# Kernel tuning notes

Measured on AMD Instinct MI355X. Metric: run time of the kernel, lower is better.

Reference implementation:

```python
import jax, jax.numpy as jnp
import numpy as np

TEMPERATURE = 0.1
EPS_NORM = 1e-12  # torch F.normalize eps
EPS_LOSS = 1e-8


def setup_inputs() -> dict:
    key = jax.random.key(0)
    k1, k2 = jax.random.split(key)
    N, D, K = 8192, 512, 64
    features = jax.random.normal(k1, (N, D), dtype=jnp.float32)
    cluster_assignments = jax.random.randint(k2, (N,), 0, K, dtype=jnp.int64)
    return {"features": features, "cluster_assignments": cluster_assignments}


def reference(features, cluster_assignments):
    # L2 normalize rows (torch.nn.functional.normalize, p=2, dim=1)
    norm = jnp.linalg.norm(features, axis=1, keepdims=True)
    features_norm = features / jnp.maximum(norm, EPS_NORM)
    # pairwise cosine similarity scaled by temperature -> [N, N]
    sim = jnp.einsum('id,jd->ij', features_norm, features_norm) / TEMPERATURE
    exp_sim = jnp.exp(sim)
    mask = (cluster_assignments[None, :] == cluster_assignments[:, None]).astype(exp_sim.dtype)
    pos_sum = jnp.sum(exp_sim * mask, axis=1, keepdims=True)
    neg_sum = jnp.sum(exp_sim * (1.0 - mask), axis=1, keepdims=True)
    loss = -jnp.log(pos_sum / (pos_sum + neg_sum + EPS_LOSS))
    return jnp.sum(loss)  # reduction='sum'
```

## Files before the change

kernel.cpp:

```cpp
#include <hip/hip_runtime.h>
#include <hip/hip_bf16.h>
#include <stdint.h>

#define N 8192
#define D 512
#define TILE 128
#define BK 64
#define NKC (D / BK)
#define NTB (N / TILE)
#define NBLK (NTB * (NTB + 1) / 2)
#define PANEL_BYTES (TILE * D)
#define KCHUNK_BYTES (TILE * BK)

typedef long long i64;
typedef __attribute__((ext_vector_type(4))) float f32x4;

__device__ __forceinline__ void gload_lds16(const void* gp, const void* lp) {
    auto g = (const __attribute__((address_space(1))) void*)(uintptr_t)gp;
    auto l = (__attribute__((address_space(3))) void*)(uintptr_t)lp;
    __builtin_amdgcn_global_load_lds(g, l, 16, 0, 0);
}

__global__ void cc_normalize(const float* __restrict__ F, uint8_t* __restrict__ Fn2,
                             float* __restrict__ out) {
    if (blockIdx.x == 0 && threadIdx.x == 0) out[0] = 0.0f;
    const int row  = blockIdx.x * 4 + (threadIdx.x >> 6);
    const int lane = threadIdx.x & 63;
    const float* p = F + (size_t)row * D + lane * 8;
    float4 a = *(const float4*)p;
    float4 b = *(const float4*)(p + 4);
    float ss = a.x*a.x + a.y*a.y + a.z*a.z + a.w*a.w
             + b.x*b.x + b.y*b.y + b.z*b.z + b.w*b.w;
    #pragma unroll
    for (int m = 32; m; m >>= 1) ss += __shfl_xor(ss, m, 64);
    const float inv = 16.0f / fmaxf(sqrtf(ss), 1e-12f);
    int lo = 0, hi = 0;
    lo = __builtin_amdgcn_cvt_pk_fp8_f32(a.x*inv, a.y*inv, lo, false);
    lo = __builtin_amdgcn_cvt_pk_fp8_f32(a.z*inv, a.w*inv, lo, true);
    hi = __builtin_amdgcn_cvt_pk_fp8_f32(b.x*inv, b.y*inv, hi, false);
    hi = __builtin_amdgcn_cvt_pk_fp8_f32(b.z*inv, b.w*inv, hi, true);
    const size_t idx = (size_t)(row >> 7) * PANEL_BYTES + (size_t)lane * 1024 + (row & 127) * 8;
    *(int2*)(Fn2 + idx) = make_int2(lo, hi);
}

__global__ __launch_bounds__(256, 3)
void cc_gemm(const uint8_t* __restrict__ Fn2, const int* __restrict__ cl,
             float* __restrict__ Pt, float* __restrict__ Pp) {
    __shared__ __align__(16) uint8_t smem[6 * KCHUNK_BYTES];
    __shared__ int crow[TILE], ccol[TILE];
    uint8_t* As = smem;
    uint8_t* Bs = smem + 3 * KCHUNK_BYTES;
    float2 (*rsum)[TILE] = (float2 (*)[TILE])(smem);
    float2 (*csum)[TILE] = (float2 (*)[TILE])(smem + 4096);

    const int tid  = threadIdx.x;
    const int wave = tid >> 6;
    const int lane = tid & 63;

    int rem = blockIdx.x, bm = 0;
    while (rem >= NTB - bm) { rem -= NTB - bm; ++bm; }
    const int bn = bm + rem;
    const bool diag = (bm == bn);

    if (tid < TILE)            crow[tid]        = cl[bm * TILE + tid];
    else                       ccol[tid - TILE] = cl[bn * TILE + (tid - TILE)];

    const int wr = wave >> 1, wc = wave & 1;
    const int q   = lane >> 4;
    const int n15 = lane & 15;

    f32x4 acc[4][4];
    #pragma unroll
    for (int t = 0; t < 4; ++t)
        #pragma unroll
        for (int u = 0; u < 4; ++u) acc[t][u] = (f32x4)(0.0f);

    const uint8_t* Ag = Fn2 + (size_t)bm * PANEL_BYTES;
    const uint8_t* Bg = Fn2 + (size_t)bn * PANEL_BYTES;

    auto stage = [&](int kc, int buf) {
        const uint8_t* ga = Ag + kc * KCHUNK_BYTES;
        const uint8_t* gb = Bg + kc * KCHUNK_BYTES;
        #pragma unroll
        for (int i = 0; i < 2; ++i) {
            const int off = (wave * 2 + i) * 1024;
            gload_lds16(ga + off + lane * 16, As + buf * KCHUNK_BYTES + off);
            gload_lds16(gb + off + lane * 16, Bs + buf * KCHUNK_BYTES + off);
        }
    };

    stage(0, 0);
    stage(1, 1);

    #pragma unroll
    for (int kc = 0; kc < NKC; ++kc) {
        const int b = kc % 3;
        if (kc < NKC - 1)
            asm volatile("s_waitcnt vmcnt(4) lgkmcnt(0)\n\ts_barrier" ::: "memory");
        else
            asm volatile("s_waitcnt vmcnt(0) lgkmcnt(0)\n\ts_barrier" ::: "memory");
        if (kc + 2 < NKC) stage(kc + 2, (kc + 2) % 3);
        #pragma unroll
        for (int ks = 0; ks < 2; ++ks) {
            const int base = b * KCHUNK_BYTES + ks * 4096 + q * 1024 + n15 * 8;
            i64 af[4], bfr[4];
            #pragma unroll
            for (int t = 0; t < 4; ++t)
                af[t] = *(const i64*)&As[base + (wr * 64 + t * 16) * 8];
            #pragma unroll
            for (int u = 0; u < 4; ++u)
                bfr[u] = *(const i64*)&Bs[base + (wc * 64 + u * 16) * 8];
            #pragma unroll
            for (int t = 0; t < 4; ++t)
                #pragma unroll
                for (int u = 0; u < 4; ++u)
                    acc[t][u] = __builtin_amdgcn_mfma_f32_16x16x32_fp8_fp8(af[t], bfr[u], acc[t][u], 0, 0, 0);
        }
    }

    __syncthreads();

    const float SC = 0.05635527503472514f;
    int cc[4];
    #pragma unroll
    for (int u = 0; u < 4; ++u) cc[u] = ccol[wc * 64 + u * 16 + n15];

    float ra[16], rp[16];
    float ce[4] = {0.f, 0.f, 0.f, 0.f};
    float cp2[4] = {0.f, 0.f, 0.f, 0.f};

    #pragma unroll
    for (int t = 0; t < 4; ++t) {
        #pragma unroll
        for (int r = 0; r < 4; ++r) {
            const int myc = crow[wr * 64 + t * 16 + q * 4 + r];
            float te = 0.0f, tp = 0.0f;
            #pragma unroll
            for (int u = 0; u < 4; ++u) {
                const float e  = exp2f(acc[t][u][r] * SC);
                const float ep = (cc[u] == myc) ? e : 0.0f;
                te += e;  tp += ep;
                ce[u] += e;  cp2[u] += ep;
            }
            ra[t * 4 + r] = te;  rp[t * 4 + r] = tp;
        }
    }

    {
        int len = 16;
        #pragma unroll
        for (int m = 1; m <= 8; m <<= 1) {
            const int half = len >> 1;
            const bool hiL = (lane & m) != 0;
            #pragma unroll
            for (int j = 0; j < half; ++j) {
                float sa = hiL ? ra[j] : ra[j + half];
                float sp = hiL ? rp[j] : rp[j + half];
                sa = __shfl_xor(sa, m, 64);
                sp = __shfl_xor(sp, m, 64);
                ra[j] = (hiL ? ra[j + half] : ra[j]) + sa;
                rp[j] = (hiL ? rp[j + half] : rp[j]) + sp;
            }
            len = half;
        }
        const int idx = ((n15 & 1) << 3) | ((n15 & 2) << 1) | ((n15 & 4) >> 1) | ((n15 & 8) >> 3);
        const int row = wr * 64 + (idx >> 2) * 16 + q * 4 + (idx & 3);
        rsum[wc][row] = make_float2(ra[0], rp[0]);
    }

    if (!diag) {
        int len = 4;
        #pragma unroll
        for (int m = 16; m <= 32; m <<= 1) {
            const int half = len >> 1;
            const bool hiL = (lane & m) != 0;
            #pragma unroll
            for (int j = 0; j < half; ++j) {
                float se = hiL ? ce[j] : ce[j + half];
                float sp = hiL ? cp2[j] : cp2[j + half];
                se = __shfl_xor(se, m, 64);
                sp = __shfl_xor(sp, m, 64);
                ce[j] = (hiL ? ce[j + half] : ce[j]) + se;
                cp2[j] = (hiL ? cp2[j + half] : cp2[j]) + sp;
            }
            len = half;
        }
        const int u = (((lane >> 4) & 1) << 1) | ((lane >> 5) & 1);
        const int col = wc * 64 + u * 16 + n15;
        csum[wr][col] = make_float2(ce[0], cp2[0]);
    }

    __syncthreads();
    if (tid < TILE) {
        const float2 r0 = rsum[0][tid], r1 = rsum[1][tid];
        const size_t o = (size_t)bn * N + bm * TILE + tid;
        Pt[o] = r0.x + r1.x;  Pp[o] = r0.y + r1.y;
    } else if (!diag) {
        const int c = tid - TILE;
        const float2 c0 = csum[0][c], c1 = csum[1][c];
        const size_t o = (size_t)bm * N + bn * TILE + c;
        Pt[o] = c0.x + c1.x;  Pp[o] = c0.y + c1.y;
    }
}

__global__ void cc_finalize(const float* __restrict__ Pt, const float* __restrict__ Pp,
                            float* __restrict__ out) {
    __shared__ float red[4];
    const int i = blockIdx.x * 256 + threadIdx.x;
    float tv = 0.0f, pv = 0.0f;
    #pragma unroll 8
    for (int s = 0; s < NTB; ++s) {
        tv += Pt[(size_t)s * N + i];
        pv += Pp[(size_t)s * N + i];
    }
    float l = __logf(tv + 1e-8f) - __logf(pv);
    #pragma unroll
    for (int m = 32; m; m >>= 1) l += __shfl_xor(l, m, 64);
    const int wv = threadIdx.x >> 6, lane = threadIdx.x & 63;
    if (lane == 0) red[wv] = l;
    __syncthreads();
    if (threadIdx.x == 0) atomicAdd(out, red[0] + red[1] + red[2] + red[3]);
}

extern "C" void kernel_launch(void* const* d_in, const int* in_sizes, int n_in,
                              void* d_out, int out_size, void* d_ws, size_t ws_size,
                              hipStream_t stream) {
    const float* F  = (const float*)d_in[0];
    const int*   cl = (const int*)d_in[1];
    float* out = (float*)d_out;

    uint8_t* Fn2 = (uint8_t*)d_ws;
    float* Pt  = (float*)((char*)d_ws + (size_t)N * D);
    float* Pp  = Pt + (size_t)NTB * N;

    cc_normalize<<<N / 4, 256, 0, stream>>>(F, Fn2, out);
    cc_gemm<<<NBLK, 256, 0, stream>>>(Fn2, cl, Pt, Pp);
    cc_finalize<<<N / 256, 256, 0, stream>>>(Pt, Pp, out);
}
```

Baseline: 111.6 us.

## Switch Gram GEMM from FP8 to INT8 MFMA with per-row rescale factors

Quantizes normalized rows to int8 (scale 127) instead of fp8, storing a per-row correction factor derived from the quantized norm. The GEMM uses the 16x16x64 i8 MFMA with 16-byte fragments, halving the MFMA instruction count per k-chunk, and changes the LDS layout to match. The epilogue rescales integer dot products by the row and column factors before exp2. This adds a small workspace array and extra loads. It relies on int8 quantization error staying acceptable for the loss.

```diff
diff --git a/kernel.cpp b/kernel.cpp
--- a/kernel.cpp
+++ b/kernel.cpp
@@ -12,8 +12,7 @@
 #define PANEL_BYTES (TILE * D)
 #define KCHUNK_BYTES (TILE * BK)
 
-typedef long long i64;
-typedef __attribute__((ext_vector_type(4))) float f32x4;
+typedef __attribute__((ext_vector_type(4))) int v4i;
 
 __device__ __forceinline__ void gload_lds16(const void* gp, const void* lp) {
     auto g = (const __attribute__((address_space(1))) void*)(uintptr_t)gp;
@@ -22,7 +21,7 @@
 }
 
 __global__ void cc_normalize(const float* __restrict__ F, uint8_t* __restrict__ Fn2,
-                             float* __restrict__ out) {
+                             float* __restrict__ g, float* __restrict__ out) {
     if (blockIdx.x == 0 && threadIdx.x == 0) out[0] = 0.0f;
     const int row  = blockIdx.x * 4 + (threadIdx.x >> 6);
     const int lane = threadIdx.x & 63;
@@ -33,21 +32,38 @@
              + b.x*b.x + b.y*b.y + b.z*b.z + b.w*b.w;
     #pragma unroll
     for (int m = 32; m; m >>= 1) ss += __shfl_xor(ss, m, 64);
-    const float inv = 16.0f / fmaxf(sqrtf(ss), 1e-12f);
-    int lo = 0, hi = 0;
-    lo = __builtin_amdgcn_cvt_pk_fp8_f32(a.x*inv, a.y*inv, lo, false);
-    lo = __builtin_amdgcn_cvt_pk_fp8_f32(a.z*inv, a.w*inv, lo, true);
-    hi = __builtin_amdgcn_cvt_pk_fp8_f32(b.x*inv, b.y*inv, hi, false);
-    hi = __builtin_amdgcn_cvt_pk_fp8_f32(b.z*inv, b.w*inv, hi, true);
-    const size_t idx = (size_t)(row >> 7) * PANEL_BYTES + (size_t)lane * 1024 + (row & 127) * 8;
-    *(int2*)(Fn2 + idx) = make_int2(lo, hi);
+    const float inv = 127.0f / fmaxf(sqrtf(ss), 1e-12f);
+
+    int qv[8];
+    qv[0] = __float2int_rn(a.x * inv);  qv[1] = __float2int_rn(a.y * inv);
+    qv[2] = __float2int_rn(a.z * inv);  qv[3] = __float2int_rn(a.w * inv);
+    qv[4] = __float2int_rn(b.x * inv);  qv[5] = __float2int_rn(b.y * inv);
+    qv[6] = __float2int_rn(b.z * inv);  qv[7] = __float2int_rn(b.w * inv);
+
+    int sq = 0;
+    #pragma unroll
+    for (int i = 0; i < 8; ++i) sq += qv[i] * qv[i];
+    #pragma unroll
+    for (int m = 32; m; m >>= 1) sq += __shfl_xor(sq, m, 64);
+    if (lane == 0)
+        g[row] = 3.7982825268f * __frsqrt_rn((float)sq);
+
+    const uint32_t lo = (uint32_t)((qv[0] & 255) | ((qv[1] & 255) << 8)
+                       | ((qv[2] & 255) << 16) | ((qv[3] & 255) << 24));
+    const uint32_t hi = (uint32_t)((qv[4] & 255) | ((qv[5] & 255) << 8)
+                       | ((qv[6] & 255) << 16) | ((qv[7] & 255) << 24));
+    const size_t idx = (size_t)(row >> 7) * PANEL_BYTES + (size_t)(lane >> 3) * 8192
+                     + (size_t)((lane >> 1) & 3) * 2048 + (row & 127) * 16 + (lane & 1) * 8;
+    *(uint2*)(Fn2 + idx) = make_uint2(lo, hi);
 }
 
 __global__ __launch_bounds__(256, 3)
 void cc_gemm(const uint8_t* __restrict__ Fn2, const int* __restrict__ cl,
+             const float* __restrict__ g,
              float* __restrict__ Pt, float* __restrict__ Pp) {
     __shared__ __align__(16) uint8_t smem[6 * KCHUNK_BYTES];
     __shared__ int crow[TILE], ccol[TILE];
+    __shared__ float gr[TILE], gc[TILE];
     uint8_t* As = smem;
     uint8_t* Bs = smem + 3 * KCHUNK_BYTES;
     float2 (*rsum)[TILE] = (float2 (*)[TILE])(smem);
@@ -62,18 +78,18 @@
     const int bn = bm + rem;
     const bool diag = (bm == bn);
 
-    if (tid < TILE)            crow[tid]        = cl[bm * TILE + tid];
-    else                       ccol[tid - TILE] = cl[bn * TILE + (tid - TILE)];
+    if (tid < TILE) { crow[tid] = cl[bm * TILE + tid];  gr[tid] = g[bm * TILE + tid]; }
+    else { const int c = tid - TILE;  ccol[c] = cl[bn * TILE + c];  gc[c] = g[bn * TILE + c]; }
 
     const int wr = wave >> 1, wc = wave & 1;
     const int q   = lane >> 4;
     const int n15 = lane & 15;
 
-    f32x4 acc[4][4];
+    v4i acc[4][4];
     #pragma unroll
     for (int t = 0; t < 4; ++t)
         #pragma unroll
-        for (int u = 0; u < 4; ++u) acc[t][u] = (f32x4)(0.0f);
+        for (int u = 0; u < 4; ++u) acc[t][u] = (v4i)(0);
 
     const uint8_t* Ag = Fn2 + (size_t)bm * PANEL_BYTES;
     const uint8_t* Bg = Fn2 + (size_t)bn * PANEL_BYTES;
@@ -100,30 +116,29 @@
         else
             asm volatile("s_waitcnt vmcnt(0) lgkmcnt(0)\n\ts_barrier" ::: "memory");
         if (kc + 2 < NKC) stage(kc + 2, (kc + 2) % 3);
-        #pragma unroll
-        for (int ks = 0; ks < 2; ++ks) {
-            const int base = b * KCHUNK_BYTES + ks * 4096 + q * 1024 + n15 * 8;
-            i64 af[4], bfr[4];
-            #pragma unroll
-            for (int t = 0; t < 4; ++t)
-                af[t] = *(const i64*)&As[base + (wr * 64 + t * 16) * 8];
+        const int base = b * KCHUNK_BYTES + q * 2048 + n15 * 16;
+        v4i af[4], bfr[4];
+        #pragma unroll
+        for (int t = 0; t < 4; ++t)
+            af[t] = *(const v4i*)&As[base + (wr * 64 + t * 16) * 16];
+        #pragma unroll
+        for (int u = 0; u < 4; ++u)
+            bfr[u] = *(const v4i*)&Bs[base + (wc * 64 + u * 16) * 16];
+        #pragma unroll
+        for (int t = 0; t < 4; ++t)
             #pragma unroll
             for (int u = 0; u < 4; ++u)
-                bfr[u] = *(const i64*)&Bs[base + (wc * 64 + u * 16) * 8];
-            #pragma unroll
-            for (int t = 0; t < 4; ++t)
-                #pragma unroll
-                for (int u = 0; u < 4; ++u)
-                    acc[t][u] = __builtin_amdgcn_mfma_f32_16x16x32_fp8_fp8(af[t], bfr[u], acc[t][u], 0, 0, 0);
-        }
+                acc[t][u] = __builtin_amdgcn_mfma_i32_16x16x64_i8(af[t], bfr[u], acc[t][u], 0, 0, 0);
     }
 
     __syncthreads();
 
-    const float SC = 0.05635527503472514f;
-    int cc[4];
-    #pragma unroll
-    for (int u = 0; u < 4; ++u) cc[u] = ccol[wc * 64 + u * 16 + n15];
+    int cc[4];  float gcu[4];
+    #pragma unroll
+    for (int u = 0; u < 4; ++u) {
+        const int c = wc * 64 + u * 16 + n15;
+        cc[u] = ccol[c];  gcu[u] = gc[c];
+    }
 
     float ra[16], rp[16];
     float ce[4] = {0.f, 0.f, 0.f, 0.f};
@@ -133,11 +148,13 @@
     for (int t = 0; t < 4; ++t) {
         #pragma unroll
         for (int r = 0; r < 4; ++r) {
-            const int myc = crow[wr * 64 + t * 16 + q * 4 + r];
+            const int lr  = wr * 64 + t * 16 + q * 4 + r;
+            const int myc = crow[lr];
+            const float g_r = gr[lr];
             float te = 0.0f, tp = 0.0f;
             #pragma unroll
             for (int u = 0; u < 4; ++u) {
-                const float e  = exp2f(acc[t][u][r] * SC);
+                const float e  = exp2f((float)acc[t][u][r] * (g_r * gcu[u]));
                 const float ep = (cc[u] == myc) ? e : 0.0f;
                 te += e;  tp += ep;
                 ce[u] += e;  cp2[u] += ep;
@@ -232,8 +249,9 @@
     uint8_t* Fn2 = (uint8_t*)d_ws;
     float* Pt  = (float*)((char*)d_ws + (size_t)N * D);
     float* Pp  = Pt + (size_t)NTB * N;
-
-    cc_normalize<<<N / 4, 256, 0, stream>>>(F, Fn2, out);
-    cc_gemm<<<NBLK, 256, 0, stream>>>(Fn2, cl, Pt, Pp);
+    float* g   = Pp + (size_t)NTB * N;
+
+    cc_normalize<<<N / 4, 256, 0, stream>>>(F, Fn2, g, out);
+    cc_gemm<<<NBLK, 256, 0, stream>>>(Fn2, cl, g, Pt, Pp);
     cc_finalize<<<N / 256, 256, 0, stream>>>(Pt, Pp, out);
 }
```

After: 142.1 us. +27.3%, slower.
